# Kernel tuning notes

Hardware: AMD Instinct MI355X
Metric: run time of the kernel (lower is better)

## Reference

```python
import jax, jax.numpy as jnp
import numpy as np
from jax import lax

N_QUBITS = 4


def _ry_gate(t):
    # t: scalar or [N] -> gate [...,2,2] (real rotation, cast to complex)
    c, s = jnp.cos(t / 2), jnp.sin(t / 2)
    return jnp.stack([jnp.stack([c, -s], -1), jnp.stack([s, c], -1)], -2).astype(jnp.complex64)


def _rx_gate(t):
    c = jnp.cos(t / 2).astype(jnp.complex64)
    s = (-1j * jnp.sin(t / 2)).astype(jnp.complex64)
    return jnp.stack([jnp.stack([c, s], -1), jnp.stack([s, c], -1)], -2)


def _rz_gate(t):
    em = jnp.exp(-1j * t / 2).astype(jnp.complex64)
    ep = jnp.exp(1j * t / 2).astype(jnp.complex64)
    z = jnp.zeros_like(em)
    return jnp.stack([jnp.stack([em, z], -1), jnp.stack([z, ep], -1)], -2)


def _apply_1q(state, gate, wire):
    # state: [N,2,2,2,2]; gate: [2,2] (shared) or [N,2,2] (batched)
    st = jnp.moveaxis(state, 1 + wire, 1)
    if gate.ndim == 2:
        new = jnp.einsum('ab,nb...->na...', gate, st)
    else:
        new = jnp.einsum('nab,nb...->na...', gate, st)
    return jnp.moveaxis(new, 1, 1 + wire)


def _apply_cnot(state, ctrl, tgt):
    st = jnp.moveaxis(state, (1 + ctrl, 1 + tgt), (1, 2))  # [N,2,2,...]
    new = jnp.stack([st[:, 0], st[:, 1, ::-1]], axis=1)
    return jnp.moveaxis(new, (1, 2), (1 + ctrl, 1 + tgt))


def _quanv_features(data, theta):
    # data: [N,4] angles per patch; returns PauliZ expvals [N,4]
    N = data.shape[0]
    state = jnp.zeros((N, 16), jnp.complex64).at[:, 0].set(1.0).reshape(N, 2, 2, 2, 2)
    # encoder: ry(data[:, w]) on wire w (batched angles)
    for w in range(N_QUBITS):
        state = _apply_1q(state, _ry_gate(data[:, w]), w)
    # fixed 'RandomLayer' of 8 ops (deterministic representative circuit)
    state = _apply_1q(state, _ry_gate(theta[0]), 0)
    state = _apply_1q(state, _rx_gate(theta[1]), 1)
    state = _apply_1q(state, _rz_gate(theta[2]), 2)
    state = _apply_cnot(state, 0, 1)
    state = _apply_1q(state, _ry_gate(theta[3]), 3)
    state = _apply_cnot(state, 2, 3)
    state = _apply_1q(state, _rx_gate(theta[4]), 0)
    state = _apply_1q(state, _rz_gate(theta[5]), 3)
    # MeasureAll(PauliZ): expval_q = P(bit_q=0) - P(bit_q=1)
    probs = jnp.abs(state) ** 2  # [N,2,2,2,2] real
    meas = []
    for q in range(N_QUBITS):
        axes = tuple(a for a in range(1, 5) if a != 1 + q)
        p = probs.sum(axes)  # [N,2]
        meas.append(p[:, 0] - p[:, 1])
    return jnp.stack(meas, -1)  # [N,4]


def setup_inputs() -> dict:
    key = jax.random.key(0)
    k1, k2, k3, k4, k5 = jax.random.split(key, 5)
    B = 2048
    x = jax.random.normal(k1, (B, 1, 56, 56), jnp.float32)
    conv_w = jax.random.normal(k2, (1, 1, 2, 2), jnp.float32) * 0.5
    theta = jax.random.uniform(k3, (6,), jnp.float32, 0.0, 2.0 * np.pi)
    W = jax.random.normal(k4, (10, 784), jnp.float32) * 0.03
    b = jax.random.normal(k5, (10,), jnp.float32) * 0.01
    return {"x": x, "conv_w": conv_w, "theta": theta, "W": W, "b": b}


def reference(x, conv_w, theta, W, b):
    B = x.shape[0]
    # classical 2x2/stride-2 conv (no bias): [B,1,56,56] -> [B,1,28,28]
    y = lax.conv_general_dilated(x, conv_w, (2, 2), 'VALID',
                                 dimension_numbers=('NCHW', 'OIHW', 'NCHW'))
    patches = y.reshape(B, -1, 4)            # [B,196,4] groups of 4 conv outputs
    P = patches.shape[1]
    data = patches.reshape(B * P, 4)
    meas = _quanv_features(data, theta)      # [B*P,4]
    feats = meas.reshape(B, P * 4)           # [B,784]
    logits = feats @ W.T + b
    return jax.nn.log_softmax(logits, axis=-1)
```

## Files before the change

kernel.cpp:

```cpp
#include <hip/hip_runtime.h>
#include <math.h>


__global__ __launch_bounds__(256) void quanv_fused(
    const float* __restrict__ x,
    const float* __restrict__ cw,
    const float* __restrict__ theta,
    const float* __restrict__ W,
    const float* __restrict__ bias,
    float* __restrict__ out,
    int B)
{
    const int wave = threadIdx.x >> 6;
    const int lane = threadIdx.x & 63;
    const int b    = blockIdx.x * 4 + wave;
    if (b >= B) return;

    const float w00 = cw[0], w01 = cw[1], w10 = cw[2], w11 = cw[3];
    const float th0  = theta[0];
    const float cth1 = cosf(theta[1]);
    const float th3  = theta[3];
    const float cth4 = cosf(theta[4]);

    float lg[10];
#pragma unroll
    for (int k = 0; k < 10; ++k) lg[k] = 0.f;

    const float* xb = x + (size_t)b * 3136;

#pragma unroll
    for (int i = 0; i < 4; ++i) {
        const int p = lane + i * 64;
        if (p < 196) {
            const int r  = p / 7;
            const int c8 = (p % 7) * 8;
            const float* xr = xb + r * 112 + c8;
            const float4 a0 = *(const float4*)(xr);
            const float4 a1 = *(const float4*)(xr + 4);
            const float4 b0 = *(const float4*)(xr + 56);
            const float4 b1 = *(const float4*)(xr + 60);

            const float d0 = w00*a0.x + w01*a0.y + w10*b0.x + w11*b0.y;
            const float d1 = w00*a0.z + w01*a0.w + w10*b0.z + w11*b0.w;
            const float d2 = w00*a1.x + w01*a1.y + w10*b1.x + w11*b1.y;
            const float d3 = w00*a1.z + w01*a1.w + w10*b1.z + w11*b1.w;

            const float c0 = cosf(d0 + th0);
            const float m0 = cth4 * c0;
            const float m1 = cth1 * c0 * cosf(d1);
            const float m2 = cosf(d2);
            const float m3 = m2 * cosf(d3 + th3);

            const float* wp = W + p * 4;
#pragma unroll
            for (int k = 0; k < 10; ++k) {
                const float4 wk = *(const float4*)(wp + k * 784);
                lg[k] += m0*wk.x + m1*wk.y + m2*wk.z + m3*wk.w;
            }
        }
    }

#pragma unroll
    for (int off = 32; off >= 1; off >>= 1) {
#pragma unroll
        for (int k = 0; k < 10; ++k)
            lg[k] += __shfl_down(lg[k], off, 64);
    }

    if (lane == 0) {
        float v[10];
        float mx = -1e30f;
#pragma unroll
        for (int k = 0; k < 10; ++k) {
            v[k] = lg[k] + bias[k];
            mx = fmaxf(mx, v[k]);
        }
        float s = 0.f;
#pragma unroll
        for (int k = 0; k < 10; ++k) s += expf(v[k] - mx);
        const float lse = mx + logf(s);
        float* ob = out + (size_t)b * 10;
#pragma unroll
        for (int k = 0; k < 10; ++k) ob[k] = v[k] - lse;
    }
}

extern "C" void kernel_launch(void* const* d_in, const int* in_sizes, int n_in,
                              void* d_out, int out_size, void* d_ws, size_t ws_size,
                              hipStream_t stream) {
    const float* x     = (const float*)d_in[0];
    const float* cw    = (const float*)d_in[1];
    const float* theta = (const float*)d_in[2];
    const float* W     = (const float*)d_in[3];
    const float* bias  = (const float*)d_in[4];
    float* out = (float*)d_out;

    const int B = in_sizes[0] / 3136;
    quanv_fused<<<(B + 3) / 4, 256, 0, stream>>>(x, cw, theta, W, bias, out, B);
}
```

Before: 79.21 us.

## Map one sample per block with per-patch threads and shared-memory reduction

```diff
diff --git a/kernel.cpp b/kernel.cpp
--- a/kernel.cpp
+++ b/kernel.cpp
@@ -11,52 +11,49 @@
     float* __restrict__ out,
     int B)
 {
-    const int wave = threadIdx.x >> 6;
-    const int lane = threadIdx.x & 63;
-    const int b    = blockIdx.x * 4 + wave;
-    if (b >= B) return;
+    const int b    = blockIdx.x;
+    const int t    = threadIdx.x;
+    const int wave = t >> 6;
+    const int lane = t & 63;
 
-    const float w00 = cw[0], w01 = cw[1], w10 = cw[2], w11 = cw[3];
-    const float th0  = theta[0];
-    const float cth1 = cosf(theta[1]);
-    const float th3  = theta[3];
-    const float cth4 = cosf(theta[4]);
+    __shared__ float red[4][10];
 
     float lg[10];
 #pragma unroll
     for (int k = 0; k < 10; ++k) lg[k] = 0.f;
 
-    const float* xb = x + (size_t)b * 3136;
+    if (t < 196) {
+        const float w00 = cw[0], w01 = cw[1], w10 = cw[2], w11 = cw[3];
+        const float th0  = theta[0];
+        const float cth1 = __cosf(theta[1]);
+        const float th3  = theta[3];
+        const float cth4 = __cosf(theta[4]);
 
+        const float* xb = x + (size_t)b * 3136;
+        const int r  = t / 7;
+        const int c8 = (t % 7) * 8;
+        const float* xr = xb + r * 112 + c8;
+        const float4 a0 = *(const float4*)(xr);
+        const float4 a1 = *(const float4*)(xr + 4);
+        const float4 b0 = *(const float4*)(xr + 56);
+        const float4 b1 = *(const float4*)(xr + 60);
+
+        const float d0 = w00*a0.x + w01*a0.y + w10*b0.x + w11*b0.y;
+        const float d1 = w00*a0.z + w01*a0.w + w10*b0.z + w11*b0.w;
+        const float d2 = w00*a1.x + w01*a1.y + w10*b1.x + w11*b1.y;
+        const float d3 = w00*a1.z + w01*a1.w + w10*b1.z + w11*b1.w;
+
+        const float c0 = __cosf(d0 + th0);
+        const float m0 = cth4 * c0;
+        const float m1 = cth1 * c0 * __cosf(d1);
+        const float m2 = __cosf(d2);
+        const float m3 = m2 * __cosf(d3 + th3);
+
+        const float* wp = W + t * 4;
 #pragma unroll
-    for (int i = 0; i < 4; ++i) {
-        const int p = lane + i * 64;
-        if (p < 196) {
-            const int r  = p / 7;
-            const int c8 = (p % 7) * 8;
-            const float* xr = xb + r * 112 + c8;
-            const float4 a0 = *(const float4*)(xr);
-            const float4 a1 = *(const float4*)(xr + 4);
-            const float4 b0 = *(const float4*)(xr + 56);
-            const float4 b1 = *(const float4*)(xr + 60);
-
-            const float d0 = w00*a0.x + w01*a0.y + w10*b0.x + w11*b0.y;
-            const float d1 = w00*a0.z + w01*a0.w + w10*b0.z + w11*b0.w;
-            const float d2 = w00*a1.x + w01*a1.y + w10*b1.x + w11*b1.y;
-            const float d3 = w00*a1.z + w01*a1.w + w10*b1.z + w11*b1.w;
-
-            const float c0 = cosf(d0 + th0);
-            const float m0 = cth4 * c0;
-            const float m1 = cth1 * c0 * cosf(d1);
-            const float m2 = cosf(d2);
-            const float m3 = m2 * cosf(d3 + th3);
-
-            const float* wp = W + p * 4;
-#pragma unroll
-            for (int k = 0; k < 10; ++k) {
-                const float4 wk = *(const float4*)(wp + k * 784);
-                lg[k] += m0*wk.x + m1*wk.y + m2*wk.z + m3*wk.w;
-            }
+        for (int k = 0; k < 10; ++k) {
+            const float4 wk = *(const float4*)(wp + k * 784);
+            lg[k] += m0*wk.x + m1*wk.y + m2*wk.z + m3*wk.w;
         }
     }
 
@@ -68,11 +65,17 @@
     }
 
     if (lane == 0) {
+#pragma unroll
+        for (int k = 0; k < 10; ++k) red[wave][k] = lg[k];
+    }
+    __syncthreads();
+
+    if (t == 0) {
         float v[10];
         float mx = -1e30f;
 #pragma unroll
         for (int k = 0; k < 10; ++k) {
-            v[k] = lg[k] + bias[k];
+            v[k] = red[0][k] + red[1][k] + red[2][k] + red[3][k] + bias[k];
             mx = fmaxf(mx, v[k]);
         }
         float s = 0.f;
@@ -96,5 +99,5 @@
     float* out = (float*)d_out;
 
     const int B = in_sizes[0] / 3136;
-    quanv_fused<<<(B + 3) / 4, 256, 0, stream>>>(x, cw, theta, W, bias, out, B);
+    quanv_fused<<<B, 256, 0, stream>>>(x, cw, theta, W, bias, out, B);
 }
```

New measurement: 78.30 us. Within noise of the previous version (-1.1%).
